# Optimization experiments

Measured on AMD Instinct MI355X. Metric: run time of the kernel, lower is better.

The kernel has to match this reference:

```python
import jax, jax.numpy as jnp
import numpy as np

EPS = 1e-8

def setup_inputs() -> dict:
    key = jax.random.key(0)
    k0, k1, k2, k3, k4 = jax.random.split(key, 5)
    B, N, K, Q, L, F = 8, 5, 5, 4, 128, 768
    support_emb = jax.random.normal(k0, (B, N, K, L, F), dtype=jnp.float32)
    query_emb = jax.random.normal(k1, (B, N * Q, L, F), dtype=jnp.float32)
    B_mask = jax.random.randint(k2, (B, N, K, L), 0, 2, dtype=jnp.int32)
    I_mask = jax.random.randint(k3, (B, N, K, L), 0, 2, dtype=jnp.int32)
    trigger_label = jax.random.randint(k4, (B, N * Q, L), 0, 2 * N + 1, dtype=jnp.int32)
    return {"support_emb": support_emb, "query_emb": query_emb, "B_mask": B_mask,
            "I_mask": I_mask, "trigger_label": trigger_label, "N": N, "K": K, "Q": Q}

def _proto(support_emb, Bm, Im, N):
    # support_emb: (B,N,K,L,F); Bm/Im: (B,N,K,L) float
    sum_B = jnp.einsum('bnklf,bnkl->bnf', support_emb, Bm)
    cnt_B = Bm.sum((2, 3))[..., None] + EPS
    pB = sum_B / cnt_B                                   # (B,N,F)
    sum_I = jnp.einsum('bnklf,bnkl->bnf', support_emb, Im)
    cnt_I = Im.sum((2, 3))[..., None] + EPS
    pI = sum_I / cnt_I                                   # (B,N,F)
    Om = 1.0 - Bm - Im                                   # (B,N,K,L)
    sum_O = jnp.einsum('bnklf,bnkl->bf', support_emb, Om)
    cnt_O = Om.sum((1, 2, 3))[:, None] + EPS
    pO = sum_O / cnt_O                                   # (B,F)
    Bsz, F = pO.shape
    # interleave: tags [O, B_0, I_0, B_1, I_1, ...]
    pBI = jnp.stack([pB, pI], axis=2).reshape(Bsz, 2 * N, F)
    return jnp.concatenate([pO[:, None, :], pBI], axis=1)  # (B, 2N+1, F)

def reference(support_emb, query_emb, B_mask, I_mask, trigger_label, N, K, Q):
    dt = support_emb.dtype
    Bm = B_mask.astype(dt)
    Im = I_mask.astype(dt)
    prototype = _proto(support_emb, Bm, Im, N)             # (B, 2N+1, F)
    # similarity: broadcast dot product -> batched GEMM
    logits = jnp.einsum('bqlf,btf->bqlt', query_emb, prototype)  # (B, NQ, L, 2N+1)
    T = logits.shape[-1]
    flat = logits.reshape(-1, T)
    pred = jnp.argmax(flat, axis=1)
    lab = trigger_label.reshape(-1)
    logp = jax.nn.log_softmax(flat, axis=-1)
    loss = -jnp.take_along_axis(logp, lab[:, None], axis=1).mean()
    return (loss, logits, pred)
```

## Files before the change

### kernel.cpp

```cpp
#include <hip/hip_runtime.h>
#include <cstdint>
#include <cstddef>

#define EPS 1e-8f

#define Bsz 8
#define Nn  5
#define Kk  5
#define Ll  128
#define Ff  768
#define Tt  11
#define KL  640
#define ROWS_PER_B 2560
#define NROWS 20480
#define F4  192
#define BN  40

#define S1_ROWS 16
#define S1_CH   (KL / S1_ROWS)
#define S1_NBLK (BN * S1_CH)
#define PART_STRIDE (3 * Ff)
#define PART_STRIDE4 (PART_STRIDE / 4)

typedef float v2f __attribute__((ext_vector_type(2)));

__global__ __launch_bounds__(192) void stage1(
    const float* __restrict__ sup,
    const int*   __restrict__ Bm,
    const int*   __restrict__ Im,
    float* __restrict__ part,
    float* __restrict__ pcnt)
{
    int blk = blockIdx.x;
    int bn  = blk / S1_CH;
    int ch  = blk - bn * S1_CH;
    int tid = threadIdx.x;

    const float4* sp = (const float4*)(sup + ((size_t)bn * KL + ch * S1_ROWS) * Ff) + tid;
    const int*    bp = Bm + bn * KL + ch * S1_ROWS;
    const int*    ip = Im + bn * KL + ch * S1_ROWS;

    v2f tB0 = {0.f,0.f}, tB1 = tB0, tI0 = tB0, tI1 = tB0, tA0 = tB0, tA1 = tB0;
    int cB = 0, cI = 0;

    #pragma unroll
    for (int h = 0; h < 2; ++h) {
        float4 v[8];
        #pragma unroll
        for (int j = 0; j < 8; ++j) v[j] = sp[(h * 8 + j) * F4];
        #pragma unroll
        for (int j = 0; j < 8; ++j) {
            int p = h * 8 + j;
            v2f lo = {v[j].x, v[j].y};
            v2f hi = {v[j].z, v[j].w};
            tA0 += lo; tA1 += hi;
            if (bp[p]) { tB0 += lo; tB1 += hi; ++cB; }
            if (ip[p]) { tI0 += lo; tI1 += hi; ++cI; }
        }
    }

    float4* o = (float4*)(part + (size_t)blk * PART_STRIDE);
    float4 rB = {tB0.x, tB0.y, tB1.x, tB1.y};
    float4 rI = {tI0.x, tI0.y, tI1.x, tI1.y};
    float4 rA = {tA0.x, tA0.y, tA1.x, tA1.y};
    o[tid]          = rB;
    o[F4 + tid]     = rI;
    o[2 * F4 + tid] = rA;

    if (tid == 0) {
        pcnt[2 * (size_t)blk]     = (float)cB;
        pcnt[2 * (size_t)blk + 1] = (float)cI;
    }
}

__global__ __launch_bounds__(256) void stage2(
    const float* __restrict__ part,
    float* __restrict__ bnsum,
    float* __restrict__ loss_out)
{
    int gid = blockIdx.x * 256 + threadIdx.x;
    if (gid == 0) loss_out[0] = 0.0f;

    int bn  = gid / (3 * F4);
    int r   = gid - bn * (3 * F4);
    int set = r / F4;
    int f4  = r - set * F4;

    const float4* src = (const float4*)(part + (size_t)bn * S1_CH * PART_STRIDE + set * Ff) + f4;
    float4 s = {0, 0, 0, 0};
    #pragma unroll
    for (int c8 = 0; c8 < S1_CH / 8; ++c8) {
        float4 v[8];
        #pragma unroll
        for (int j = 0; j < 8; ++j) v[j] = src[(size_t)(c8 * 8 + j) * PART_STRIDE4];
        #pragma unroll
        for (int j = 0; j < 8; ++j) {
            s.x += v[j].x; s.y += v[j].y; s.z += v[j].z; s.w += v[j].w;
        }
    }
    ((float4*)bnsum)[((size_t)bn * 3 + set) * F4 + f4] = s;
}

#define S3_ROWS 64
#define S3_NBLK (NROWS / S3_ROWS)
#define BLKS_PER_B (ROWS_PER_B / S3_ROWS)

__global__ __launch_bounds__(128) void stage3(
    const float* __restrict__ query,
    const float* __restrict__ bnsum,
    const float* __restrict__ pcnt,
    const int*   __restrict__ label,
    float* __restrict__ out_logits,
    float* __restrict__ out_pred,
    float* __restrict__ loss_out)
{
    __shared__ float4 ldsP[Tt * 4 * 49];
    __shared__ float  sCnt[2 * Nn];
    __shared__ float  sScale[Tt];

    int blk = blockIdx.x;
    int b   = blk / BLKS_PER_B;
    int tid = threadIdx.x;

    if (tid < 2 * Nn) sCnt[tid] = 0.0f;
    __syncthreads();
    for (int i = tid; i < 400; i += 128) {
        float v = pcnt[400 * b + i];
        int n   = i / 80;
        int set = i & 1;
        atomicAdd(&sCnt[2 * n + set], v);
    }
    __syncthreads();
    if (tid < Tt) {
        if (tid == 0) {
            float cO = (float)(KL * Nn);
            #pragma unroll
            for (int k = 0; k < 2 * Nn; ++k) cO -= sCnt[k];
            sScale[0] = 1.0f / (cO + EPS);
        } else {
            sScale[tid] = 1.0f / (sCnt[tid - 1] + EPS);
        }
    }
    __syncthreads();

    const float4* bs = (const float4*)bnsum + (size_t)b * Nn * 3 * F4;
    for (int idx = tid; idx < Tt * F4; idx += 128) {
        int t  = idx / F4;
        int f4 = idx - t * F4;
        float4 val;
        if (t == 0) {
            float sx = 0, sy = 0, sz = 0, sw = 0;
            #pragma unroll
            for (int n = 0; n < Nn; ++n) {
                float4 A = bs[(n * 3 + 2) * F4 + f4];
                float4 Bv = bs[(n * 3 + 0) * F4 + f4];
                float4 Iv = bs[(n * 3 + 1) * F4 + f4];
                sx += A.x - Bv.x - Iv.x; sy += A.y - Bv.y - Iv.y;
                sz += A.z - Bv.z - Iv.z; sw += A.w - Bv.w - Iv.w;
            }
            val.x = sx; val.y = sy; val.z = sz; val.w = sw;
        } else {
            int n   = (t - 1) >> 1;
            int set = (t - 1) & 1;
            val = bs[(n * 3 + set) * F4 + f4];
        }
        float sc = sScale[t];
        val.x *= sc; val.y *= sc; val.z *= sc; val.w *= sc;
        int s = f4 / 48, j = f4 - 48 * s;
        ldsP[(t * 4 + s) * 49 + j] = val;
    }
    __syncthreads();

    int w    = tid >> 6;
    int lane = tid & 63;
    int p    = lane >> 2;
    int s    = lane & 3;

    size_t row0 = (size_t)blk * S3_ROWS + w * 32 + p * 2;
    const float4* q0 = (const float4*)(query + row0 * Ff) + s * 48;
    const float4* q1 = q0 + F4;

    float a0[Tt], a1[Tt];
    #pragma unroll
    for (int t = 0; t < Tt; ++t) { a0[t] = 0.0f; a1[t] = 0.0f; }

    const float4* pb = &ldsP[s * 49];
    #pragma unroll 2
    for (int j = 0; j < 48; ++j) {
        float4 u = q0[j];
        float4 v = q1[j];
        #pragma unroll
        for (int t = 0; t < Tt; ++t) {
            float4 pv = pb[t * (4 * 49) + j];
            float d0 = a0[t], d1 = a1[t];
            d0 = fmaf(u.x, pv.x, d0); d0 = fmaf(u.y, pv.y, d0);
            d0 = fmaf(u.z, pv.z, d0); d0 = fmaf(u.w, pv.w, d0);
            d1 = fmaf(v.x, pv.x, d1); d1 = fmaf(v.y, pv.y, d1);
            d1 = fmaf(v.z, pv.z, d1); d1 = fmaf(v.w, pv.w, d1);
            a0[t] = d0; a1[t] = d1;
        }
    }

    #pragma unroll
    for (int t = 0; t < Tt; ++t) {
        a0[t] += __shfl_xor(a0[t], 1, 64); a0[t] += __shfl_xor(a0[t], 2, 64);
        a1[t] += __shfl_xor(a1[t], 1, 64); a1[t] += __shfl_xor(a1[t], 2, 64);
    }

    float wloss = 0.0f;
    if (s == 0) {
        #pragma unroll
        for (int rr = 0; rr < 2; ++rr) {
            size_t grow = row0 + rr;
            float* a = rr ? a1 : a0;
            float m = a[0]; int bt = 0;
            #pragma unroll
            for (int t = 1; t < Tt; ++t) if (a[t] > m) { m = a[t]; bt = t; }
            float sum = 0.0f;
            #pragma unroll
            for (int t = 0; t < Tt; ++t) sum += __expf(a[t] - m);
            int lab = label[grow];
            float labv = a[0];
            #pragma unroll
            for (int t = 1; t < Tt; ++t) labv = (lab == t) ? a[t] : labv;
            #pragma unroll
            for (int t = 0; t < Tt; ++t) out_logits[grow * Tt + t] = a[t];
            out_pred[grow] = (float)bt;
            wloss += (m + __logf(sum)) - labv;
        }
    }
    #pragma unroll
    for (int off = 32; off > 0; off >>= 1) wloss += __shfl_xor(wloss, off, 64);
    if (lane == 0) atomicAdd(loss_out, wloss * (1.0f / (float)NROWS));
}

extern "C" void kernel_launch(void* const* d_in, const int* in_sizes, int n_in,
                              void* d_out, int out_size, void* d_ws, size_t ws_size,
                              hipStream_t stream) {
    const float* sup   = (const float*)d_in[0];
    const float* query = (const float*)d_in[1];
    const int*   Bm    = (const int*)d_in[2];
    const int*   Im    = (const int*)d_in[3];
    const int*   lab   = (const int*)d_in[4];

    float* w     = (float*)d_ws;
    float* part  = w;
    float* pcnt  = part + (size_t)S1_NBLK * PART_STRIDE;
    float* bnsum = pcnt + 2 * S1_NBLK;

    float* loss_out   = (float*)d_out;
    float* out_logits = (float*)d_out + 1;
    float* out_pred   = (float*)d_out + 1 + (size_t)NROWS * Tt;

    stage1<<<S1_NBLK, 192, 0, stream>>>(sup, Bm, Im, part, pcnt);
    stage2<<<90, 256, 0, stream>>>(part, bnsum, loss_out);
    stage3<<<S3_NBLK, 128, 0, stream>>>(query, bnsum, pcnt, lab,
                                        out_logits, out_pred, loss_out);
}
```

Measured before the change: 201.8 us.

## Split prototype build into separate kernel and restructure reduction and GEMM stages

Stage2 now reduces partials with 768-thread blocks (one per bn/set) using shared-memory tree reduction and also folds the mask counts. A new stage2b builds normalized prototypes once, so stage3 no longer recomputes the counts and prototypes in every block and just copies them into LDS. Stage3 is remapped to 16 lanes per row pair with coalesced strided query loads, 32 rows per block, 256 threads and all query loads issued up front. This adds one kernel launch and higher register pressure in exchange for less redundant per-block setup and better memory access.

New measurement: 217.9 us. 8.0% more time.

```diff
diff --git a/kernel.cpp b/kernel.cpp
--- a/kernel.cpp
+++ b/kernel.cpp
@@ -73,165 +73,189 @@
     }
 }
 
-__global__ __launch_bounds__(256) void stage2(
+__global__ __launch_bounds__(768) void stage2(
     const float* __restrict__ part,
+    const float* __restrict__ pcnt,
     float* __restrict__ bnsum,
+    float* __restrict__ cnt,
     float* __restrict__ loss_out)
 {
-    int gid = blockIdx.x * 256 + threadIdx.x;
-    if (gid == 0) loss_out[0] = 0.0f;
-
-    int bn  = gid / (3 * F4);
-    int r   = gid - bn * (3 * F4);
-    int set = r / F4;
-    int f4  = r - set * F4;
-
-    const float4* src = (const float4*)(part + (size_t)bn * S1_CH * PART_STRIDE + set * Ff) + f4;
+    __shared__ float4 red[768];
+
+    int blk = blockIdx.x;
+    int bn  = blk / 3;
+    int set = blk - bn * 3;
+    int tid = threadIdx.x;
+
+    if (blk == 0 && tid == 0) loss_out[0] = 0.0f;
+
+    int q  = tid / F4;
+    int f4 = tid - q * F4;
+
+    const float4* src = (const float4*)part + ((size_t)bn * 3 * S1_CH + set) * F4 + f4;
     float4 s = {0, 0, 0, 0};
-    #pragma unroll
-    for (int c8 = 0; c8 < S1_CH / 8; ++c8) {
-        float4 v[8];
-        #pragma unroll
-        for (int j = 0; j < 8; ++j) v[j] = src[(size_t)(c8 * 8 + j) * PART_STRIDE4];
-        #pragma unroll
-        for (int j = 0; j < 8; ++j) {
-            s.x += v[j].x; s.y += v[j].y; s.z += v[j].z; s.w += v[j].w;
+    float4 v[10];
+    #pragma unroll
+    for (int k = 0; k < 10; ++k) v[k] = src[(size_t)(q * 10 + k) * PART_STRIDE4];
+    #pragma unroll
+    for (int k = 0; k < 10; ++k) {
+        s.x += v[k].x; s.y += v[k].y; s.z += v[k].z; s.w += v[k].w;
+    }
+    red[tid] = s;
+
+    if (set < 2 && tid < 64) {
+        float cv = (tid < S1_CH) ? pcnt[2 * ((size_t)bn * S1_CH + tid) + set] : 0.0f;
+        #pragma unroll
+        for (int off = 32; off > 0; off >>= 1) cv += __shfl_xor(cv, off, 64);
+        if (tid == 0) cnt[2 * bn + set] = cv;
+    }
+
+    __syncthreads();
+    if (q == 0) {
+        float4 a = red[f4];
+        float4 b = red[F4 + f4];
+        float4 c = red[2 * F4 + f4];
+        float4 d = red[3 * F4 + f4];
+        float4 t4 = {a.x + b.x + c.x + d.x, a.y + b.y + c.y + d.y,
+                     a.z + b.z + c.z + d.z, a.w + b.w + c.w + d.w};
+        ((float4*)bnsum)[((size_t)bn * 3 + set) * F4 + f4] = t4;
+    }
+}
+
+__global__ __launch_bounds__(192) void stage2b(
+    const float* __restrict__ bnsum,
+    const float* __restrict__ cnt,
+    float* __restrict__ proto)
+{
+    int b  = blockIdx.x / Tt;
+    int t  = blockIdx.x - b * Tt;
+    int f4 = threadIdx.x;
+
+    const float4* bs = (const float4*)bnsum + (size_t)b * Nn * 3 * F4;
+
+    float scale;
+    if (t == 0) {
+        float cO = (float)(KL * Nn);
+        #pragma unroll
+        for (int k = 0; k < 2 * Nn; ++k) cO -= cnt[2 * Nn * b + k];
+        scale = 1.0f / (cO + EPS);
+    } else {
+        scale = 1.0f / (cnt[2 * Nn * b + (t - 1)] + EPS);
+    }
+
+    float4 val;
+    if (t == 0) {
+        float sx = 0, sy = 0, sz = 0, sw = 0;
+        #pragma unroll
+        for (int n = 0; n < Nn; ++n) {
+            float4 A  = bs[(n * 3 + 2) * F4 + f4];
+            float4 Bv = bs[(n * 3 + 0) * F4 + f4];
+            float4 Iv = bs[(n * 3 + 1) * F4 + f4];
+            sx += A.x - Bv.x - Iv.x; sy += A.y - Bv.y - Iv.y;
+            sz += A.z - Bv.z - Iv.z; sw += A.w - Bv.w - Iv.w;
         }
-    }
-    ((float4*)bnsum)[((size_t)bn * 3 + set) * F4 + f4] = s;
-}
-
-#define S3_ROWS 64
+        val.x = sx; val.y = sy; val.z = sz; val.w = sw;
+    } else {
+        int n  = (t - 1) >> 1;
+        int st = (t - 1) & 1;
+        val = bs[(n * 3 + st) * F4 + f4];
+    }
+    val.x *= scale; val.y *= scale; val.z *= scale; val.w *= scale;
+    ((float4*)proto)[((size_t)b * Tt + t) * F4 + f4] = val;
+}
+
+#define S3_ROWS 32
 #define S3_NBLK (NROWS / S3_ROWS)
-#define BLKS_PER_B (ROWS_PER_B / S3_ROWS)
-
-__global__ __launch_bounds__(128) void stage3(
+#define S3_BPB  (ROWS_PER_B / S3_ROWS)
+
+#define DOT_STEP(JV, UU, WW)                                              \
+    {                                                                     \
+        _Pragma("unroll")                                                 \
+        for (int t = 0; t < Tt; ++t) {                                    \
+            float4 pv = pb[t * F4 + (JV) * 16];                           \
+            float d0 = a0[t], d1 = a1[t];                                 \
+            d0 = fmaf((UU).x, pv.x, d0); d0 = fmaf((UU).y, pv.y, d0);     \
+            d0 = fmaf((UU).z, pv.z, d0); d0 = fmaf((UU).w, pv.w, d0);     \
+            d1 = fmaf((WW).x, pv.x, d1); d1 = fmaf((WW).y, pv.y, d1);     \
+            d1 = fmaf((WW).z, pv.z, d1); d1 = fmaf((WW).w, pv.w, d1);     \
+            a0[t] = d0; a1[t] = d1;                                       \
+        }                                                                 \
+    }
+
+__global__ __launch_bounds__(256, 3) void stage3(
     const float* __restrict__ query,
-    const float* __restrict__ bnsum,
-    const float* __restrict__ pcnt,
+    const float* __restrict__ proto,
     const int*   __restrict__ label,
     float* __restrict__ out_logits,
     float* __restrict__ out_pred,
     float* __restrict__ loss_out)
 {
-    __shared__ float4 ldsP[Tt * 4 * 49];
-    __shared__ float  sCnt[2 * Nn];
-    __shared__ float  sScale[Tt];
+    __shared__ float4 ldsP[Tt * F4];
 
     int blk = blockIdx.x;
-    int b   = blk / BLKS_PER_B;
+    int b   = blk / S3_BPB;
     int tid = threadIdx.x;
 
-    if (tid < 2 * Nn) sCnt[tid] = 0.0f;
+    const float4* pp = (const float4*)proto + (size_t)b * Tt * F4;
+    for (int idx = tid; idx < Tt * F4; idx += 256) ldsP[idx] = pp[idx];
     __syncthreads();
-    for (int i = tid; i < 400; i += 128) {
-        float v = pcnt[400 * b + i];
-        int n   = i / 80;
-        int set = i & 1;
-        atomicAdd(&sCnt[2 * n + set], v);
-    }
-    __syncthreads();
-    if (tid < Tt) {
-        if (tid == 0) {
-            float cO = (float)(KL * Nn);
-            #pragma unroll
-            for (int k = 0; k < 2 * Nn; ++k) cO -= sCnt[k];
-            sScale[0] = 1.0f / (cO + EPS);
-        } else {
-            sScale[tid] = 1.0f / (sCnt[tid - 1] + EPS);
-        }
-    }
-    __syncthreads();
-
-    const float4* bs = (const float4*)bnsum + (size_t)b * Nn * 3 * F4;
-    for (int idx = tid; idx < Tt * F4; idx += 128) {
-        int t  = idx / F4;
-        int f4 = idx - t * F4;
-        float4 val;
-        if (t == 0) {
-            float sx = 0, sy = 0, sz = 0, sw = 0;
-            #pragma unroll
-            for (int n = 0; n < Nn; ++n) {
-                float4 A = bs[(n * 3 + 2) * F4 + f4];
-                float4 Bv = bs[(n * 3 + 0) * F4 + f4];
-                float4 Iv = bs[(n * 3 + 1) * F4 + f4];
-                sx += A.x - Bv.x - Iv.x; sy += A.y - Bv.y - Iv.y;
-                sz += A.z - Bv.z - Iv.z; sw += A.w - Bv.w - Iv.w;
-            }
-            val.x = sx; val.y = sy; val.z = sz; val.w = sw;
-        } else {
-            int n   = (t - 1) >> 1;
-            int set = (t - 1) & 1;
-            val = bs[(n * 3 + set) * F4 + f4];
-        }
-        float sc = sScale[t];
-        val.x *= sc; val.y *= sc; val.z *= sc; val.w *= sc;
-        int s = f4 / 48, j = f4 - 48 * s;
-        ldsP[(t * 4 + s) * 49 + j] = val;
-    }
-    __syncthreads();
-
-    int w    = tid >> 6;
-    int lane = tid & 63;
-    int p    = lane >> 2;
-    int s    = lane & 3;
-
-    size_t row0 = (size_t)blk * S3_ROWS + w * 32 + p * 2;
-    const float4* q0 = (const float4*)(query + row0 * Ff) + s * 48;
+
+    int p = tid >> 4;
+    int s = tid & 15;
+
+    size_t row0 = (size_t)blk * S3_ROWS + p * 2;
+    const float4* q0 = (const float4*)query + row0 * F4 + s;
     const float4* q1 = q0 + F4;
 
     float a0[Tt], a1[Tt];
     #pragma unroll
     for (int t = 0; t < Tt; ++t) { a0[t] = 0.0f; a1[t] = 0.0f; }
 
-    const float4* pb = &ldsP[s * 49];
-    #pragma unroll 2
-    for (int j = 0; j < 48; ++j) {
-        float4 u = q0[j];
-        float4 v = q1[j];
-        #pragma unroll
-        for (int t = 0; t < Tt; ++t) {
-            float4 pv = pb[t * (4 * 49) + j];
-            float d0 = a0[t], d1 = a1[t];
-            d0 = fmaf(u.x, pv.x, d0); d0 = fmaf(u.y, pv.y, d0);
-            d0 = fmaf(u.z, pv.z, d0); d0 = fmaf(u.w, pv.w, d0);
-            d1 = fmaf(v.x, pv.x, d1); d1 = fmaf(v.y, pv.y, d1);
-            d1 = fmaf(v.z, pv.z, d1); d1 = fmaf(v.w, pv.w, d1);
-            a0[t] = d0; a1[t] = d1;
-        }
-    }
+    float4 u0[6], w0[6], u1[6], w1[6];
+    #pragma unroll
+    for (int j = 0; j < 6; ++j) { u0[j] = q0[j * 16]; w0[j] = q1[j * 16]; }
+    #pragma unroll
+    for (int j = 0; j < 6; ++j) { u1[j] = q0[(j + 6) * 16]; w1[j] = q1[(j + 6) * 16]; }
+
+    const float4* pb = ldsP + s;
+    #pragma unroll
+    for (int j = 0; j < 6; ++j) DOT_STEP(j, u0[j], w0[j]);
+    #pragma unroll
+    for (int j = 0; j < 6; ++j) DOT_STEP(j + 6, u1[j], w1[j]);
 
     #pragma unroll
     for (int t = 0; t < Tt; ++t) {
-        a0[t] += __shfl_xor(a0[t], 1, 64); a0[t] += __shfl_xor(a0[t], 2, 64);
-        a1[t] += __shfl_xor(a1[t], 1, 64); a1[t] += __shfl_xor(a1[t], 2, 64);
+        a0[t] += __shfl_xor(a0[t], 1, 16); a0[t] += __shfl_xor(a0[t], 2, 16);
+        a0[t] += __shfl_xor(a0[t], 4, 16); a0[t] += __shfl_xor(a0[t], 8, 16);
+        a1[t] += __shfl_xor(a1[t], 1, 16); a1[t] += __shfl_xor(a1[t], 2, 16);
+        a1[t] += __shfl_xor(a1[t], 4, 16); a1[t] += __shfl_xor(a1[t], 8, 16);
     }
 
     float wloss = 0.0f;
-    if (s == 0) {
-        #pragma unroll
-        for (int rr = 0; rr < 2; ++rr) {
-            size_t grow = row0 + rr;
-            float* a = rr ? a1 : a0;
-            float m = a[0]; int bt = 0;
-            #pragma unroll
-            for (int t = 1; t < Tt; ++t) if (a[t] > m) { m = a[t]; bt = t; }
-            float sum = 0.0f;
-            #pragma unroll
-            for (int t = 0; t < Tt; ++t) sum += __expf(a[t] - m);
-            int lab = label[grow];
-            float labv = a[0];
-            #pragma unroll
-            for (int t = 1; t < Tt; ++t) labv = (lab == t) ? a[t] : labv;
-            #pragma unroll
-            for (int t = 0; t < Tt; ++t) out_logits[grow * Tt + t] = a[t];
-            out_pred[grow] = (float)bt;
-            wloss += (m + __logf(sum)) - labv;
-        }
+    if (s < 2) {
+        float rv[Tt];
+        #pragma unroll
+        for (int t = 0; t < Tt; ++t) rv[t] = s ? a1[t] : a0[t];
+        size_t grow = row0 + s;
+
+        float m = rv[0]; int bt = 0;
+        #pragma unroll
+        for (int t = 1; t < Tt; ++t) if (rv[t] > m) { m = rv[t]; bt = t; }
+        float sum = 0.0f;
+        #pragma unroll
+        for (int t = 0; t < Tt; ++t) sum += __expf(rv[t] - m);
+        int lab = label[grow];
+        float labv = rv[0];
+        #pragma unroll
+        for (int t = 1; t < Tt; ++t) labv = (lab == t) ? rv[t] : labv;
+        #pragma unroll
+        for (int t = 0; t < Tt; ++t) out_logits[grow * Tt + t] = rv[t];
+        out_pred[grow] = (float)bt;
+        wloss = (m + __logf(sum)) - labv;
     }
     #pragma unroll
     for (int off = 32; off > 0; off >>= 1) wloss += __shfl_xor(wloss, off, 64);
-    if (lane == 0) atomicAdd(loss_out, wloss * (1.0f / (float)NROWS));
+    if ((tid & 63) == 0) atomicAdd(loss_out, wloss * (1.0f / (float)NROWS));
 }
 
 extern "C" void kernel_launch(void* const* d_in, const int* in_sizes, int n_in,
@@ -247,13 +271,16 @@
     float* part  = w;
     float* pcnt  = part + (size_t)S1_NBLK * PART_STRIDE;
     float* bnsum = pcnt + 2 * S1_NBLK;
+    float* cnt   = bnsum + (size_t)BN * 3 * Ff;
+    float* proto = cnt + 2 * BN;
 
     float* loss_out   = (float*)d_out;
     float* out_logits = (float*)d_out + 1;
     float* out_pred   = (float*)d_out + 1 + (size_t)NROWS * Tt;
 
     stage1<<<S1_NBLK, 192, 0, stream>>>(sup, Bm, Im, part, pcnt);
-    stage2<<<90, 256, 0, stream>>>(part, bnsum, loss_out);
-    stage3<<<S3_NBLK, 128, 0, stream>>>(query, bnsum, pcnt, lab,
+    stage2<<<3 * BN, 768, 0, stream>>>(part, pcnt, bnsum, cnt, loss_out);
+    stage2b<<<Bsz * Tt, 192, 0, stream>>>(bnsum, cnt, proto);
+    stage3<<<S3_NBLK, 256, 0, stream>>>(query, proto, lab,
                                         out_logits, out_pred, loss_out);
 }
```
